# Optimization experiments

Measured on AMD Instinct MI355X. Metric: run time of the kernel, lower is better.

## Reference

```python
import jax, jax.numpy as jnp
import numpy as np

EPS = 1e-10
TEMP = 0.01
THETA = 0.1
BETA = 1.0
GAMMA = 1.0  # FocalLoss(gamma=1)
N, C = 32768, 1000


def setup_inputs() -> dict:
    key = jax.random.key(0)
    k1, k2, k3 = jax.random.split(key, 3)
    probs = jax.random.uniform(k1, (N, C), dtype=jnp.float32)
    probs = probs / jnp.sum(probs, axis=1, keepdims=True)  # valid distributions
    lbl = jax.random.randint(k2, (N,), 0, C)
    y = jax.nn.one_hot(lbl, C, dtype=jnp.float32)
    weights = jax.random.uniform(k3, (N, C), dtype=jnp.float32)
    return {"probs": probs, "y": y, "weights": weights}


def _entropy(p):
    return -jnp.sum(p * jnp.log(jnp.clip(p, EPS)), axis=1)


def _soft_T(e):
    num = e * (1.0 - THETA)
    den = jnp.clip((1.0 - e) * THETA, EPS)
    v = (1.0 / TEMP) * jnp.log(jnp.clip(num / den, EPS))
    return jax.nn.sigmoid(v)


def reference(probs, y, weights):
    num_classes = probs.shape[1]
    entmax = jnp.log(jnp.float32(num_classes))

    predictions = jnp.argmax(probs, axis=1)          # [N]
    labels = jnp.argmax(y)                            # scalar (faithful to original)
    unc = _entropy(probs)                             # [N]

    th_list = jnp.linspace(0.0, 1.0, 21, dtype=jnp.float32)
    umin, umax = jnp.min(unc), jnp.max(unc)
    unc_th = umin + th_list * (umax - umin)           # [21]

    acc = (predictions == labels)                     # [N] bool
    s = _soft_T(unc / entmax)                         # [N]
    t = jnp.tanh(unc)                                 # [N]
    cert_w = (1.0 - s) * (1.0 - t)                    # certain weight
    uncw = s * t                                      # uncertain weight

    le = unc[None, :] <= unc_th[:, None]              # [21, N]
    accb = acc[None, :]
    zero = jnp.float32(0.0)
    n_ac = jnp.sum(jnp.where(le & accb, cert_w[None, :], zero), axis=1)
    n_au = jnp.sum(jnp.where((~le) & accb, uncw[None, :], zero), axis=1)
    n_ic = jnp.sum(jnp.where(le & (~accb), cert_w[None, :], zero), axis=1)
    n_iu = jnp.sum(jnp.where((~le) & (~accb), uncw[None, :], zero), axis=1)

    avu = (n_ac + n_iu) / (n_ac + n_au + n_ic + n_iu + EPS)  # [21]
    # trapezoid rule over th_list (increasing -> direction = 1)
    dx = jnp.diff(th_list)
    auc_avu = jnp.sum(0.5 * (avu[1:] + avu[:-1]) * dx)

    logp = jnp.log(jnp.clip(probs, 1e-08))            # FocalLoss eps = 1e-8
    base = y * logp
    focal_loss = jnp.mean(-jnp.sum(base * weights * (1.0 - probs) ** GAMMA, axis=1))
    ce_loss = jnp.mean(-jnp.sum(base, axis=1))

    savu_loss = -BETA * jnp.log(jnp.clip(auc_avu, EPS)) + focal_loss
    return (savu_loss, ce_loss)
```

## Files before the change

### kernel.cpp

```cpp
#include <hip/hip_runtime.h>
#include <hip/hip_bf16.h>

constexpr int kN = 32768;
constexpr int kC = 1000;
constexpr int NB_A = 2048;
constexpr int NB_B = 1024;
constexpr int NB3 = 512;

__global__ __launch_bounds__(256) void k1_main(
    const float* __restrict__ probs, const float* __restrict__ y,
    const float* __restrict__ wts, float* __restrict__ unc,
    int* __restrict__ pred, float* __restrict__ partMM ,
    float* __restrict__ partCF ) {
  const int lane = threadIdx.x & 63;
  const int wid = threadIdx.x >> 6;

  if (blockIdx.x < NB_A) {
    const int gw = blockIdx.x * 4 + wid;
    float mn = 3.4e38f, mx = -3.4e38f;
#pragma unroll 1
    for (int r = 0; r < 4; ++r) {
      const int i = gw + r * 8192;
      const float* pr = probs + (size_t)i * kC;
      float4 p4[4];
#pragma unroll
      for (int k = 0; k < 4; ++k) {
        const int c0 = k * 256 + lane * 4;
        if (c0 < kC) p4[k] = *reinterpret_cast<const float4*>(pr + c0);
        else p4[k] = make_float4(0.f, 0.f, 0.f, 0.f);
      }
      float ent = 0.f, bv = -3.4e38f; int bi = 0;
#pragma unroll
      for (int k = 0; k < 4; ++k) {
        const int c0 = k * 256 + lane * 4;
#pragma unroll
        for (int j = 0; j < 4; ++j) {
          const float p = (&p4[k].x)[j];
          ent += p * __logf(fmaxf(p, 1e-10f));
          if (p > bv) { bv = p; bi = c0 + j; }
        }
      }
#pragma unroll
      for (int off = 32; off; off >>= 1) {
        ent += __shfl_xor(ent, off);
        const float bv2 = __shfl_xor(bv, off);
        const int bi2 = __shfl_xor(bi, off);
        if (bv2 > bv || (bv2 == bv && bi2 < bi)) { bv = bv2; bi = bi2; }
      }
      const float u = -ent;
      if (lane == 0) { unc[i] = u; pred[i] = bi; }
      mn = fminf(mn, u); mx = fmaxf(mx, u);
    }
    __shared__ float sMin[4], sMax[4];
    if (lane == 0) { sMin[wid] = mn; sMax[wid] = mx; }
    __syncthreads();
    if (threadIdx.x == 0) {
      float a = 3.4e38f, b = -3.4e38f;
#pragma unroll
      for (int q = 0; q < 4; ++q) { a = fminf(a, sMin[q]); b = fmaxf(b, sMax[q]); }
      partMM[blockIdx.x * 2 + 0] = a;
      partMM[blockIdx.x * 2 + 1] = b;
    }
  } else {
    const int gwb = (blockIdx.x - NB_A) * 4 + wid;
    constexpr float kLogClip8 = -18.420680743952367f;
    float ce = 0.f, fo = 0.f;
#pragma unroll 1
    for (int r = 0; r < 8; ++r) {
      const int i = gwb + r * 4096;
      const float* yr = y + (size_t)i * kC;
      int lbl = -1;
#pragma unroll 1
      for (int step = 0; step < 4; ++step) {
        const int c0 = step * 256 + lane * 4;
        float4 y4 = make_float4(0.f, 0.f, 0.f, 0.f);
        if (c0 < kC) y4 = *reinterpret_cast<const float4*>(yr + c0);
        int loc = -1;
#pragma unroll
        for (int j = 0; j < 4; ++j) if ((&y4.x)[j] != 0.0f) loc = j;
        if (__any(loc >= 0)) {
          if (loc >= 0) lbl = c0 + loc;
          break;
        }
      }
      if (lbl >= 0) {
        const float p = probs[(size_t)i * kC + lbl];
        const float w = wts[(size_t)i * kC + lbl];
        const float lp = fmaxf(__logf(fmaxf(p, 1e-10f)), kLogClip8);
        ce += lp;
        fo += lp * w * (1.0f - p);
      }
    }
#pragma unroll
    for (int off = 32; off; off >>= 1) {
      ce += __shfl_xor(ce, off);
      fo += __shfl_xor(fo, off);
    }
    __shared__ float sCe[4], sFo[4];
    if (lane == 0) { sCe[wid] = ce; sFo[wid] = fo; }
    __syncthreads();
    if (threadIdx.x == 0) {
      float c = 0.f, f = 0.f;
#pragma unroll
      for (int q = 0; q < 4; ++q) { c += sCe[q]; f += sFo[q]; }
      const int bb = blockIdx.x - NB_A;
      partCF[bb * 2 + 0] = c;
      partCF[bb * 2 + 1] = f;
    }
  }
}

__global__ __launch_bounds__(256) void k2_scalars(
    const float* __restrict__ y, const float* __restrict__ partMM,
    const float* __restrict__ partCF, float* __restrict__ scal) {
  const int t = threadIdx.x;
  float mn = 3.4e38f, mx = -3.4e38f, c = 0.f, f = 0.f;
  for (int b = t; b < NB_A; b += 256) {
    mn = fminf(mn, partMM[b * 2 + 0]);
    mx = fmaxf(mx, partMM[b * 2 + 1]);
  }
  for (int b = t; b < NB_B; b += 256) {
    c += partCF[b * 2 + 0];
    f += partCF[b * 2 + 1];
  }
  __shared__ float sc[256], sf[256], smn[256], smx[256];
  sc[t] = c; sf[t] = f; smn[t] = mn; smx[t] = mx;
  __syncthreads();
  for (int off = 128; off; off >>= 1) {
    if (t < off) {
      sc[t] += sc[t + off]; sf[t] += sf[t + off];
      smn[t] = fminf(smn[t], smn[t + off]);
      smx[t] = fmaxf(smx[t], smx[t + off]);
    }
    __syncthreads();
  }
  float bv = -3.4e38f; int bi = 0;
  for (int c0 = t; c0 < kC; c0 += 256) {
    const float v = y[c0];
    if (v > bv) { bv = v; bi = c0; }
  }
  __shared__ float sbv[256]; __shared__ int sbi[256];
  sbv[t] = bv; sbi[t] = bi;
  __syncthreads();
  for (int off = 128; off; off >>= 1) {
    if (t < off) {
      if (sbv[t + off] > sbv[t] ||
          (sbv[t + off] == sbv[t] && sbi[t + off] < sbi[t])) {
        sbv[t] = sbv[t + off]; sbi[t] = sbi[t + off];
      }
    }
    __syncthreads();
  }
  if (t == 0) {
    scal[0] = -sc[0] / (float)kN;
    scal[1] = -sf[0] / (float)kN;
    const float umin = smn[0], umax = smx[0];
    scal[2] = umin; scal[3] = umax;
    for (int k = 0; k < 21; ++k) {
      const float th = (float)((double)k * 0.05);
      scal[4 + k] = umin + th * (umax - umin);
    }
    reinterpret_cast<int*>(scal)[25] = sbi[0];
  }
}

__global__ __launch_bounds__(64) void k3_hist(
    const float* __restrict__ unc, const int* __restrict__ pred,
    const float* __restrict__ scal, float* __restrict__ part3 ) {
  __shared__ float hist[88 * 64];
  __shared__ float th[21];
  __shared__ int s_label;
  const int t = threadIdx.x;
  for (int b = 0; b < 88; ++b) hist[b * 64 + t] = 0.f;
  if (t < 21) th[t] = scal[4 + t];
  if (t == 0) s_label = reinterpret_cast<const int*>(scal)[25];
  __syncthreads();
  const float entmax = logf(1000.0f);
  const int label = s_label;

  for (int i = blockIdx.x * 64 + t; i < kN; i += NB3 * 64) {
    const float u = unc[i];
    const bool acc = (pred[i] == label);
    const float e = u / entmax;
    const float num = e * 0.9f;
    const float den = fmaxf((1.0f - e) * 0.1f, 1e-10f);
    const float v = 100.0f * logf(fmaxf(num / den, 1e-10f));
    const float s = 1.0f / (1.0f + expf(-v));
    const float tt = tanhf(u);
    const float cw = (1.0f - s) * (1.0f - tt);
    const float uw = s * tt;
    int k0 = 0;
#pragma unroll
    for (int k = 0; k < 21; ++k) k0 += (th[k] < u) ? 1 : 0;
    const int base = acc ? 0 : 44;
    hist[(base + k0) * 64 + t] += cw;
    hist[(base + 22 + k0) * 64 + t] += uw;
  }
  __syncthreads();
  for (int b = t; b < 88; b += 64) {
    float s2 = 0.f;
    for (int q = 0; q < 64; ++q) s2 += hist[b * 64 + q];
    part3[blockIdx.x * 88 + b] = s2;
  }
}

__global__ __launch_bounds__(128) void k4_final(
    const float* __restrict__ part3, const float* __restrict__ scal,
    float* __restrict__ out) {
  __shared__ float h[88];
  const int t = threadIdx.x;
  for (int b = t; b < 88; b += 128) {
    float s = 0.f;
    for (int q = 0; q < NB3; ++q) s += part3[q * 88 + b];
    h[b] = s;
  }
  __syncthreads();
  if (t == 0) {
    float totAU = 0.f, totIU = 0.f;
    for (int k = 0; k < 22; ++k) { totAU += h[22 + k]; totIU += h[66 + k]; }
    float avu[21];
    float cAC = 0.f, cAU = 0.f, cIC = 0.f, cIU = 0.f;
    for (int k = 0; k < 21; ++k) {
      cAC += h[k]; cAU += h[22 + k]; cIC += h[44 + k]; cIU += h[66 + k];
      const float n_ac = cAC;
      const float n_au = totAU - cAU;
      const float n_ic = cIC;
      const float n_iu = totIU - cIU;
      avu[k] = (n_ac + n_iu) / (n_ac + n_au + n_ic + n_iu + 1e-10f);
    }
    float auc = 0.f;
    for (int k = 0; k < 20; ++k) {
      const float th0 = (float)((double)k * 0.05);
      const float th1 = (float)((double)(k + 1) * 0.05);
      auc += 0.5f * (avu[k + 1] + avu[k]) * (th1 - th0);
    }
    out[0] = -logf(fmaxf(auc, 1e-10f)) + scal[1];
    out[1] = scal[0];
  }
}

extern "C" void kernel_launch(void* const* d_in, const int* in_sizes, int n_in,
                              void* d_out, int out_size, void* d_ws, size_t ws_size,
                              hipStream_t stream) {
  const float* probs = (const float*)d_in[0];
  const float* y     = (const float*)d_in[1];
  const float* wts   = (const float*)d_in[2];
  float* out = (float*)d_out;

  float* ws     = (float*)d_ws;
  float* unc    = ws;
  int*   pred   = (int*)(ws + kN);
  float* partMM = ws + 2 * kN;
  float* partCF = partMM + NB_A * 2;
  float* scal   = partCF + NB_B * 2;
  float* part3  = scal + 32;

  k1_main<<<dim3(NB_A + NB_B), dim3(256), 0, stream>>>(
      probs, y, wts, unc, pred, partMM, partCF);
  k2_scalars<<<dim3(1), dim3(256), 0, stream>>>(y, partMM, partCF, scal);
  k3_hist<<<dim3(NB3), dim3(64), 0, stream>>>(unc, pred, scal, part3);
  k4_final<<<dim3(1), dim3(128), 0, stream>>>(part3, scal, out);
}
```

Before: 65.91 us.

## Fuse single-block reduction kernels into predecessors via last-block ticket

Folds the single-block scalar reduction into k1_main and the final AUC reduction into k3_hist. Each block takes an atomic ticket after a threadfence, and the last block to arrive does the reduction. This drops two kernel launches and the gaps between them. In exchange it adds a memset to reset the tickets, an atomic per block, and a serial tail run by one block.

```diff
diff --git a/kernel.cpp b/kernel.cpp
--- a/kernel.cpp
+++ b/kernel.cpp
@@ -5,15 +5,18 @@
 constexpr int kC = 1000;
 constexpr int NB_A = 2048;
 constexpr int NB_B = 1024;
+constexpr int NB1 = NB_A + NB_B;
 constexpr int NB3 = 512;
 
 __global__ __launch_bounds__(256) void k1_main(
     const float* __restrict__ probs, const float* __restrict__ y,
     const float* __restrict__ wts, float* __restrict__ unc,
     int* __restrict__ pred, float* __restrict__ partMM ,
-    float* __restrict__ partCF ) {
+    float* __restrict__ partCF , float* __restrict__ scal,
+    int* __restrict__ ticket) {
   const int lane = threadIdx.x & 63;
   const int wid = threadIdx.x >> 6;
+  __shared__ int sLast;
 
   if (blockIdx.x < NB_A) {
     const int gw = blockIdx.x * 4 + wid;
@@ -108,11 +111,16 @@
       partCF[bb * 2 + 1] = f;
     }
   }
-}
-
-__global__ __launch_bounds__(256) void k2_scalars(
-    const float* __restrict__ y, const float* __restrict__ partMM,
-    const float* __restrict__ partCF, float* __restrict__ scal) {
+
+  __syncthreads();
+  if (threadIdx.x == 0) {
+    __threadfence();
+    sLast = (atomicAdd(ticket, 1) == NB1 - 1) ? 1 : 0;
+  }
+  __syncthreads();
+  if (!sLast) return;
+  __threadfence();
+
   const int t = threadIdx.x;
   float mn = 3.4e38f, mx = -3.4e38f, c = 0.f, f = 0.f;
   for (int b = t; b < NB_A; b += 256) {
@@ -166,10 +174,11 @@
 
 __global__ __launch_bounds__(64) void k3_hist(
     const float* __restrict__ unc, const int* __restrict__ pred,
-    const float* __restrict__ scal, float* __restrict__ part3 ) {
+    const float* __restrict__ scal, float* __restrict__ part3 ,
+    float* __restrict__ out, int* __restrict__ ticket) {
   __shared__ float hist[88 * 64];
   __shared__ float th[21];
-  __shared__ int s_label;
+  __shared__ int s_label, sLast;
   const int t = threadIdx.x;
   for (int b = 0; b < 88; ++b) hist[b * 64 + t] = 0.f;
   if (t < 21) th[t] = scal[4 + t];
@@ -202,17 +211,21 @@
     for (int q = 0; q < 64; ++q) s2 += hist[b * 64 + q];
     part3[blockIdx.x * 88 + b] = s2;
   }
-}
-
-__global__ __launch_bounds__(128) void k4_final(
-    const float* __restrict__ part3, const float* __restrict__ scal,
-    float* __restrict__ out) {
+
+  __syncthreads();
+  if (t == 0) {
+    __threadfence();
+    sLast = (atomicAdd(ticket, 1) == NB3 - 1) ? 1 : 0;
+  }
+  __syncthreads();
+  if (!sLast) return;
+  __threadfence();
+
   __shared__ float h[88];
-  const int t = threadIdx.x;
-  for (int b = t; b < 88; b += 128) {
-    float s = 0.f;
-    for (int q = 0; q < NB3; ++q) s += part3[q * 88 + b];
-    h[b] = s;
+  for (int b = t; b < 88; b += 64) {
+    float s2 = 0.f;
+    for (int q = 0; q < NB3; ++q) s2 += part3[q * 88 + b];
+    h[b] = s2;
   }
   __syncthreads();
   if (t == 0) {
@@ -247,17 +260,18 @@
   const float* wts   = (const float*)d_in[2];
   float* out = (float*)d_out;
 
-  float* ws     = (float*)d_ws;
-  float* unc    = ws;
-  int*   pred   = (int*)(ws + kN);
-  float* partMM = ws + 2 * kN;
-  float* partCF = partMM + NB_A * 2;
-  float* scal   = partCF + NB_B * 2;
-  float* part3  = scal + 32;
-
-  k1_main<<<dim3(NB_A + NB_B), dim3(256), 0, stream>>>(
-      probs, y, wts, unc, pred, partMM, partCF);
-  k2_scalars<<<dim3(1), dim3(256), 0, stream>>>(y, partMM, partCF, scal);
-  k3_hist<<<dim3(NB3), dim3(64), 0, stream>>>(unc, pred, scal, part3);
-  k4_final<<<dim3(1), dim3(128), 0, stream>>>(part3, scal, out);
+  float* ws      = (float*)d_ws;
+  float* unc     = ws;
+  int*   pred    = (int*)(ws + kN);
+  float* partMM  = ws + 2 * kN;
+  float* partCF  = partMM + NB_A * 2;
+  float* scal    = partCF + NB_B * 2;
+  float* part3   = scal + 32;
+  int*   tickets = (int*)(part3 + NB3 * 88);
+
+  hipMemsetAsync(tickets, 0, 2 * sizeof(int), stream);
+  k1_main<<<dim3(NB1), dim3(256), 0, stream>>>(
+      probs, y, wts, unc, pred, partMM, partCF, scal, &tickets[0]);
+  k3_hist<<<dim3(NB3), dim3(64), 0, stream>>>(
+      unc, pred, scal, part3, out, &tickets[1]);
 }
```

After: 174.4 us. 2.65x slower.

## Drop scalar-reduction kernel via atomic min/max and fold CE reduction into final

Applied to the files above, without the earlier changes.

Removes the single-block k2_scalars kernel. The uncertainty min and max are now reduced with integer atomicMax on float bit patterns, using the complement trick for min, which holds because entropy is non-negative. The global label is taken from row 0 inside k1, and k3 computes the thresholds itself. The CE and focal partial sums are reduced in k4 instead. This saves one serialized launch and its tail latency, at the cost of a memset before k1 and some atomic contention.

```diff
diff --git a/kernel.cpp b/kernel.cpp
--- a/kernel.cpp
+++ b/kernel.cpp
@@ -10,8 +10,8 @@
 __global__ __launch_bounds__(256) void k1_main(
     const float* __restrict__ probs, const float* __restrict__ y,
     const float* __restrict__ wts, float* __restrict__ unc,
-    int* __restrict__ pred, float* __restrict__ partMM ,
-    float* __restrict__ partCF ) {
+    int* __restrict__ pred, unsigned int* __restrict__ minmax ,
+    float* __restrict__ partCF , int* __restrict__ labelOut) {
   const int lane = threadIdx.x & 63;
   const int wid = threadIdx.x >> 6;
 
@@ -58,8 +58,8 @@
       float a = 3.4e38f, b = -3.4e38f;
 #pragma unroll
       for (int q = 0; q < 4; ++q) { a = fminf(a, sMin[q]); b = fmaxf(b, sMax[q]); }
-      partMM[blockIdx.x * 2 + 0] = a;
-      partMM[blockIdx.x * 2 + 1] = b;
+      atomicMax(&minmax[0], ~__float_as_uint(a));
+      atomicMax(&minmax[1], __float_as_uint(b));
     }
   } else {
     const int gwb = (blockIdx.x - NB_A) * 4 + wid;
@@ -83,6 +83,7 @@
           break;
         }
       }
+      if (i == 0 && lbl >= 0) *labelOut = lbl;
       if (lbl >= 0) {
         const float p = probs[(size_t)i * kC + lbl];
         const float w = wts[(size_t)i * kC + lbl];
@@ -110,70 +111,24 @@
   }
 }
 
-__global__ __launch_bounds__(256) void k2_scalars(
-    const float* __restrict__ y, const float* __restrict__ partMM,
-    const float* __restrict__ partCF, float* __restrict__ scal) {
-  const int t = threadIdx.x;
-  float mn = 3.4e38f, mx = -3.4e38f, c = 0.f, f = 0.f;
-  for (int b = t; b < NB_A; b += 256) {
-    mn = fminf(mn, partMM[b * 2 + 0]);
-    mx = fmaxf(mx, partMM[b * 2 + 1]);
-  }
-  for (int b = t; b < NB_B; b += 256) {
-    c += partCF[b * 2 + 0];
-    f += partCF[b * 2 + 1];
-  }
-  __shared__ float sc[256], sf[256], smn[256], smx[256];
-  sc[t] = c; sf[t] = f; smn[t] = mn; smx[t] = mx;
-  __syncthreads();
-  for (int off = 128; off; off >>= 1) {
-    if (t < off) {
-      sc[t] += sc[t + off]; sf[t] += sf[t + off];
-      smn[t] = fminf(smn[t], smn[t + off]);
-      smx[t] = fmaxf(smx[t], smx[t + off]);
-    }
-    __syncthreads();
-  }
-  float bv = -3.4e38f; int bi = 0;
-  for (int c0 = t; c0 < kC; c0 += 256) {
-    const float v = y[c0];
-    if (v > bv) { bv = v; bi = c0; }
-  }
-  __shared__ float sbv[256]; __shared__ int sbi[256];
-  sbv[t] = bv; sbi[t] = bi;
-  __syncthreads();
-  for (int off = 128; off; off >>= 1) {
-    if (t < off) {
-      if (sbv[t + off] > sbv[t] ||
-          (sbv[t + off] == sbv[t] && sbi[t + off] < sbi[t])) {
-        sbv[t] = sbv[t + off]; sbi[t] = sbi[t + off];
-      }
-    }
-    __syncthreads();
-  }
-  if (t == 0) {
-    scal[0] = -sc[0] / (float)kN;
-    scal[1] = -sf[0] / (float)kN;
-    const float umin = smn[0], umax = smx[0];
-    scal[2] = umin; scal[3] = umax;
-    for (int k = 0; k < 21; ++k) {
-      const float th = (float)((double)k * 0.05);
-      scal[4 + k] = umin + th * (umax - umin);
-    }
-    reinterpret_cast<int*>(scal)[25] = sbi[0];
-  }
-}
-
 __global__ __launch_bounds__(64) void k3_hist(
     const float* __restrict__ unc, const int* __restrict__ pred,
-    const float* __restrict__ scal, float* __restrict__ part3 ) {
+    const unsigned int* __restrict__ minmax, const int* __restrict__ labelIn,
+    float* __restrict__ part3 ) {
   __shared__ float hist[88 * 64];
   __shared__ float th[21];
   __shared__ int s_label;
   const int t = threadIdx.x;
   for (int b = 0; b < 88; ++b) hist[b * 64 + t] = 0.f;
-  if (t < 21) th[t] = scal[4 + t];
-  if (t == 0) s_label = reinterpret_cast<const int*>(scal)[25];
+  if (t == 0) {
+    const float umin = __uint_as_float(~minmax[0]);
+    const float umax = __uint_as_float(minmax[1]);
+    for (int k = 0; k < 21; ++k) {
+      const float thf = (float)((double)k * 0.05);
+      th[k] = umin + thf * (umax - umin);
+    }
+    s_label = *labelIn;
+  }
   __syncthreads();
   const float entmax = logf(1000.0f);
   const int label = s_label;
@@ -205,17 +160,30 @@
 }
 
 __global__ __launch_bounds__(128) void k4_final(
-    const float* __restrict__ part3, const float* __restrict__ scal,
+    const float* __restrict__ part3, const float* __restrict__ partCF,
     float* __restrict__ out) {
   __shared__ float h[88];
+  __shared__ float sc[128], sf[128];
   const int t = threadIdx.x;
   for (int b = t; b < 88; b += 128) {
     float s = 0.f;
     for (int q = 0; q < NB3; ++q) s += part3[q * 88 + b];
     h[b] = s;
   }
+  float c = 0.f, f = 0.f;
+  for (int b = t; b < NB_B; b += 128) {
+    c += partCF[b * 2 + 0];
+    f += partCF[b * 2 + 1];
+  }
+  sc[t] = c; sf[t] = f;
   __syncthreads();
+  for (int off = 64; off; off >>= 1) {
+    if (t < off) { sc[t] += sc[t + off]; sf[t] += sf[t + off]; }
+    __syncthreads();
+  }
   if (t == 0) {
+    const float ce_mean = -sc[0] / (float)kN;
+    const float focal_mean = -sf[0] / (float)kN;
     float totAU = 0.f, totIU = 0.f;
     for (int k = 0; k < 22; ++k) { totAU += h[22 + k]; totIU += h[66 + k]; }
     float avu[21];
@@ -234,8 +202,8 @@
       const float th1 = (float)((double)(k + 1) * 0.05);
       auc += 0.5f * (avu[k + 1] + avu[k]) * (th1 - th0);
     }
-    out[0] = -logf(fmaxf(auc, 1e-10f)) + scal[1];
-    out[1] = scal[0];
+    out[0] = -logf(fmaxf(auc, 1e-10f)) + focal_mean;
+    out[1] = ce_mean;
   }
 }
 
@@ -247,17 +215,18 @@
   const float* wts   = (const float*)d_in[2];
   float* out = (float*)d_out;
 
-  float* ws     = (float*)d_ws;
-  float* unc    = ws;
-  int*   pred   = (int*)(ws + kN);
-  float* partMM = ws + 2 * kN;
-  float* partCF = partMM + NB_A * 2;
-  float* scal   = partCF + NB_B * 2;
-  float* part3  = scal + 32;
-
+  float* ws      = (float*)d_ws;
+  float* unc     = ws;
+  int*   pred    = (int*)(ws + kN);
+  float* partCF  = ws + 2 * kN;
+  float* part3   = partCF + NB_B * 2;
+  unsigned int* minmax = (unsigned int*)(part3 + NB3 * 88);
+  int*   labelOut = (int*)(minmax + 2);
+
+  hipMemsetAsync(minmax, 0, 2 * sizeof(unsigned int), stream);
   k1_main<<<dim3(NB_A + NB_B), dim3(256), 0, stream>>>(
-      probs, y, wts, unc, pred, partMM, partCF);
-  k2_scalars<<<dim3(1), dim3(256), 0, stream>>>(y, partMM, partCF, scal);
-  k3_hist<<<dim3(NB3), dim3(64), 0, stream>>>(unc, pred, scal, part3);
-  k4_final<<<dim3(1), dim3(128), 0, stream>>>(part3, scal, out);
-}
+      probs, y, wts, unc, pred, minmax, partCF, labelOut);
+  k3_hist<<<dim3(NB3), dim3(64), 0, stream>>>(
+      unc, pred, minmax, labelOut, part3);
+  k4_final<<<dim3(1), dim3(128), 0, stream>>>(part3, partCF, out);
+}
```

Result: slower. 101.9 us (+54.6%).
